# Kernel optimization log

Measured on AMD Instinct MI355X. Metric: run time of the kernel, lower is better.

## Reference

```python
import jax, jax.numpy as jnp
import numpy as np

B, N_IMG, D = 256, 128, 768
E, S, H = 3, 44, 1024  # S = ceil(128/3) rounded up to multiple of 4; H = 4*D//E
MAX_SLOTS = 88
LN_EPS = 1e-5


def setup_inputs() -> dict:
    key = jax.random.key(0)
    ks = jax.random.split(key, 12)
    x = jax.random.normal(ks[0], (B, N_IMG + 1, D), dtype=jnp.float32)
    attn_weight = jax.random.uniform(ks[1], (B, N_IMG), dtype=jnp.float32)
    ln_gamma = jnp.ones((D,), jnp.float32)
    ln_beta = jnp.zeros((D,), jnp.float32)
    vsg_w = jax.random.normal(ks[2], (D + 1, D), jnp.float32) / np.sqrt(D + 1)
    vsg_b = jnp.zeros((D,), jnp.float32)
    mu = jax.random.normal(ks[3], (E, D, MAX_SLOTS), jnp.float32) / np.sqrt(D)
    scale = jnp.ones((1,), jnp.float32)
    # per-expert MLP: kaiming-ish / xavier-ish random params
    w1 = jax.random.normal(ks[4], (E, D, H), jnp.float32) * np.sqrt(2.0 / D)
    b1 = jnp.zeros((E, H), jnp.float32)
    w2 = jax.random.normal(ks[5], (E, H, D), jnp.float32) * np.sqrt(2.0 / (H + D))
    b2 = jnp.zeros((E, D), jnp.float32)
    cw1 = jax.random.normal(ks[6], (D, 4 * D), jnp.float32) * np.sqrt(2.0 / D)
    cb1 = jnp.zeros((4 * D,), jnp.float32)
    cw2 = jax.random.normal(ks[7], (4 * D, D), jnp.float32) * np.sqrt(2.0 / (4 * D))
    cb2 = jnp.zeros((D,), jnp.float32)
    return dict(x=x, attn_weight=attn_weight, ln_gamma=ln_gamma, ln_beta=ln_beta,
                vsg_w=vsg_w, vsg_b=vsg_b, mu=mu, scale=scale,
                w1=w1, b1=b1, w2=w2, b2=b2, cw1=cw1, cb1=cb1, cw2=cw2, cb2=cb2)


def reference(x, attn_weight, ln_gamma, ln_beta, vsg_w, vsg_b, mu, scale,
              w1, b1, w2, b2, cw1, cb1, cw2, cb2):
    b, np1, d = x.shape
    n = np1 - 1
    img = x[:, 1:, :]            # [B, N, D]
    cls = x[:, 0, :]             # [B, D]

    # LayerNorm on image tokens
    mean = img.mean(-1, keepdims=True)
    var = img.var(-1, keepdims=True)  # biased, matches torch LayerNorm
    img_n = (img - mean) * jax.lax.rsqrt(var + LN_EPS) * ln_gamma + ln_beta

    # slot bias from [cls_feat, mean attention] -> visible_slot_gen (mode='original')
    attn_feat = attn_weight.mean(axis=1, keepdims=True)            # [B, 1]
    slot_input = jnp.concatenate([cls, attn_feat], axis=-1)        # [B, D+1]
    slot_bias = slot_input @ vsg_w + vsg_b                         # [B, D]

    # adjusted slot prototypes: mu[:, :, :S].permute(1,0,2) + slot_bias broadcast over (E, S)
    adj_mu = mu[:, :, :S].transpose(1, 0, 2)[None] + slot_bias[:, :, None, None]  # [B, D, E, S]

    logits = jnp.einsum('bnd,bdes->bnes', img_n * scale, adj_mu)   # [B, N, E, S]

    # expert group mask from attention thresholds (groups (1,1,1))
    vis = attn_weight > 0.7
    part = (attn_weight >= 0.3) & (attn_weight <= 0.7)
    occ = attn_weight < 0.3
    emask = jnp.stack([vis, part, occ], axis=-1).astype(logits.dtype)  # [B, N, E]
    logits = logits * emask[:, :, :, None]

    # softmax over tokens (dispatch) and over flattened slots (combine)
    dispatch = jax.nn.softmax(logits, axis=1)                      # [B, N, E, S]
    combine = jax.nn.softmax(logits.reshape(b, n, E * S), axis=-1) # [B, N, E*S]

    slot_in = jnp.einsum('bnd,bnes->besd', img, dispatch)          # [B, E, S, D]

    # batched per-expert MLP (fused grouped GEMM instead of python loop)
    h = jax.nn.gelu(jnp.einsum('besd,edh->besh', slot_in, w1) + b1[:, None, :],
                    approximate=False)
    slot_out = jnp.einsum('besh,ehd->besd', h, w2) + b2[:, None, :]  # [B, E, S, D]

    slot_flat = slot_out.reshape(b, E * S, d)
    img_out = jnp.einsum('bsd,bns->bnd', slot_flat, combine)       # [B, N, D]

    # CLS token through its dedicated dense MLP
    cls_h = jax.nn.gelu(cls @ cw1 + cb1, approximate=False)
    cls_out = cls_h @ cw2 + cb2                                    # [B, D]

    return jnp.concatenate([cls_out[:, None, :], img_out], axis=1)  # [B, N+1, D]
```

## Files before the change

### kernel.cpp

```cpp
#include <hip/hip_runtime.h>
#include <hip/hip_bf16.h>
#include <math.h>

#define NB   256
#define NIMG 128
#define DIM  768
#define NE   3
#define NS   44
#define NH   1024
#define ESL  132
#define NTOK (NB*NIMG)
#define MAXSLOTS 88
#define BIGI (1 << 30)
#define KPAD 160

typedef __bf16 bf16x8 __attribute__((ext_vector_type(8)));
typedef float f32x4 __attribute__((ext_vector_type(4)));
typedef const __attribute__((address_space(1))) void* gas_t;
typedef __attribute__((address_space(3))) void* las_t;

__device__ __forceinline__ float gelu_f(float v) {
    return 0.5f * v * (1.0f + erff(v * 0.70710678118654752f));
}

__device__ __forceinline__ float block_reduce_sum256(float v, float* red) {
    int tid = threadIdx.x;
    red[tid] = v;
    __syncthreads();
    for (int s = 128; s > 0; s >>= 1) {
        if (tid < s) red[tid] += red[tid + s];
        __syncthreads();
    }
    float r = red[0];
    __syncthreads();
    return r;
}

__global__ void repack_mu_k(const float* __restrict__ mu, __hip_bfloat16* __restrict__ bt) {
    int idx = blockIdx.x * 256 + threadIdx.x;
    if (idx >= 256 * DIM) return;
    int r = idx / DIM, d = idx - r * DIM;
    float v = 0.f;
    if (r < ESL) {
        int e = r / NS, s = r - e * NS;
        v = mu[((size_t)e * DIM + d) * MAXSLOTS + s];
    }
    bt[idx] = __float2bfloat16(v);
}

__global__ void transpose_bf16_k(const float* __restrict__ in, __hip_bfloat16* __restrict__ outp,
                                 int R, int Cc, long long inBS, long long outBS) {
    __shared__ float t[32][33];
    in   += (long long)blockIdx.z * inBS;
    outp += (long long)blockIdx.z * outBS;
    int c0 = blockIdx.x * 32, r0 = blockIdx.y * 32;
    int tx = threadIdx.x, ty = threadIdx.y;
    for (int i = 0; i < 32; i += 8) {
        int r = r0 + ty + i, c = c0 + tx;
        t[ty + i][tx] = (r < R && c < Cc) ? in[(size_t)r * Cc + c] : 0.f;
    }
    __syncthreads();
    for (int i = 0; i < 32; i += 8) {
        int r = c0 + ty + i, c = r0 + tx;
        if (r < Cc && c < R) outp[(size_t)r * R + c] = __float2bfloat16(t[tx][ty + i]);
    }
}

__global__ void cls_bf16_k(const float* __restrict__ x, __hip_bfloat16* __restrict__ cls16) {
    int idx = blockIdx.x * 256 + threadIdx.x;
    if (idx >= NB * DIM) return;
    int b = idx / DIM, j = idx - b * DIM;
    cls16[idx] = __float2bfloat16(x[(size_t)b * 129 * DIM + j]);
}

__global__ void zero_pad_k(__hip_bfloat16* __restrict__ p) {
    const int per = KPAD - ESL;
    const int total = NB * DIM * per;
    int idx = blockIdx.x * 256 + threadIdx.x;
    if (idx >= total) return;
    int bd = idx / per, k = idx - bd * per;
    p[(size_t)bd * KPAD + ESL + k] = __float2bfloat16(0.f);
}

__global__ void slot_bias_k(const float* __restrict__ x, const float* __restrict__ aw,
                            const float* __restrict__ vsg_w, const float* __restrict__ vsg_b,
                            float* __restrict__ slot_bias) {
    __shared__ float red[256];
    __shared__ float cls[DIM];
    int b = blockIdx.x, tid = threadIdx.x;
    float a = (tid < NIMG) ? aw[b * NIMG + tid] : 0.f;
    float af = block_reduce_sum256(a, red) * (1.0f / NIMG);
    for (int j = tid; j < DIM; j += 256) cls[j] = x[(size_t)b * 129 * DIM + j];
    __syncthreads();
    int j0 = tid, j1 = tid + 256, j2 = tid + 512;
    float acc0 = 0.f, acc1 = 0.f, acc2 = 0.f;
    for (int d = 0; d < DIM; ++d) {
        float c = cls[d];
        const float* wr = vsg_w + (size_t)d * DIM;
        acc0 = fmaf(c, wr[j0], acc0);
        acc1 = fmaf(c, wr[j1], acc1);
        acc2 = fmaf(c, wr[j2], acc2);
    }
    const float* wl = vsg_w + (size_t)DIM * DIM;
    float* out = slot_bias + (size_t)b * DIM;
    out[j0] = acc0 + vsg_b[j0] + af * wl[j0];
    out[j1] = acc1 + vsg_b[j1] + af * wl[j1];
    out[j2] = acc2 + vsg_b[j2] + af * wl[j2];
}

__global__ void ln_t2_k(const float* __restrict__ x, const float* __restrict__ gamma,
                        const float* __restrict__ beta, const float* __restrict__ slot_bias,
                        __hip_bfloat16* __restrict__ img_n, float* __restrict__ t2) {
    __shared__ float red[256];
    int tok = blockIdx.x;
    int b = tok >> 7, n = tok & 127;
    int tid = threadIdx.x;
    const float* row = x + ((size_t)b * 129 + 1 + n) * DIM;
    float v0 = row[tid], v1 = row[tid + 256], v2 = row[tid + 512];
    float s  = block_reduce_sum256(v0 + v1 + v2, red);
    float ss = block_reduce_sum256(v0*v0 + v1*v1 + v2*v2, red);
    float mean = s * (1.0f / DIM);
    float var  = ss * (1.0f / DIM) - mean * mean;
    float inv  = rsqrtf(var + 1e-5f);
    const float* sb = slot_bias + (size_t)b * DIM;
    __hip_bfloat16* orow = img_n + (size_t)tok * DIM;
    float tacc = 0.f;
    int j = tid;
    float y0 = (v0 - mean) * inv * gamma[j] + beta[j]; orow[j] = __float2bfloat16(y0); tacc = fmaf(y0, sb[j], tacc);
    j = tid + 256;
    float y1 = (v1 - mean) * inv * gamma[j] + beta[j]; orow[j] = __float2bfloat16(y1); tacc = fmaf(y1, sb[j], tacc);
    j = tid + 512;
    float y2 = (v2 - mean) * inv * gamma[j] + beta[j]; orow[j] = __float2bfloat16(y2); tacc = fmaf(y2, sb[j], tacc);
    float t = block_reduce_sum256(tacc, red);
    if (tid == 0) t2[tok] = t;
}

__global__ void mask_k(float* __restrict__ L, const float* __restrict__ t2,
                       const float* __restrict__ aw, const float* __restrict__ scale) {
    int idx = blockIdx.x * 256 + threadIdx.x;
    if (idx >= NTOK * ESL) return;
    int tok = idx / ESL, r = idx - tok * ESL;
    int e = r / NS;
    float a = aw[tok];
    int sel = (a > 0.7f) ? 0 : ((a >= 0.3f) ? 1 : 2);
    float v = 0.f;
    if (e == sel) v = scale[0] * (L[idx] + t2[tok]);
    L[idx] = v;
}

__global__ void dispatch_k(const float* __restrict__ L, __hip_bfloat16* __restrict__ dT16) {
    __shared__ float red[128];
    int es = blockIdx.x, b = blockIdx.y, tid = threadIdx.x;
    float v = L[((size_t)(b * NIMG + tid)) * ESL + es];
    red[tid] = v; __syncthreads();
    for (int s = 64; s > 0; s >>= 1) { if (tid < s) red[tid] = fmaxf(red[tid], red[tid + s]); __syncthreads(); }
    float mx = red[0]; __syncthreads();
    float e = __expf(v - mx);
    red[tid] = e; __syncthreads();
    for (int s = 64; s > 0; s >>= 1) { if (tid < s) red[tid] += red[tid + s]; __syncthreads(); }
    float sum = red[0];
    dT16[((size_t)b * ESL + es) * NIMG + tid] = __float2bfloat16(e / sum);
}

__global__ void combine_k(const float* __restrict__ L, __hip_bfloat16* __restrict__ C) {
    int tok = blockIdx.x, lane = threadIdx.x;
    const float* row = L + (size_t)tok * ESL;
    float v0 = row[lane], v1 = row[lane + 64];
    bool has2 = lane < (ESL - 128);
    float v2 = has2 ? row[lane + 128] : -1e30f;
    float m = fmaxf(fmaxf(v0, v1), v2);
    for (int o = 32; o > 0; o >>= 1) m = fmaxf(m, __shfl_xor(m, o));
    float e0 = __expf(v0 - m), e1 = __expf(v1 - m);
    float e2 = has2 ? __expf(v2 - m) : 0.f;
    float s = e0 + e1 + e2;
    for (int o = 32; o > 0; o >>= 1) s += __shfl_xor(s, o);
    float inv = 1.0f / s;
    __hip_bfloat16* orow = C + (size_t)tok * KPAD;
    orow[lane] = __float2bfloat16(e0 * inv);
    orow[lane + 64] = __float2bfloat16(e1 * inv);
    if (has2) orow[lane + 128] = __float2bfloat16(e2 * inv);
    else if (lane < KPAD - 128) orow[lane + 128] = __float2bfloat16(0.f);
}

__global__ __launch_bounds__(256)
void mfma2_k(const __hip_bfloat16* __restrict__ A_, long long aBS, int lda, int Mrows,
             const __hip_bfloat16* __restrict__ Bt_, long long bBS, int ldb, int Nrows,
             const float* __restrict__ bias, long long biasBS,
             void* __restrict__ Cv, long long cBS, int ldc, int cSub, long long cOuter,
             int Mlim, int Nlim, int K, int act, int out_bf16, int ctrans,
             int nx, int ny, int order)
{
    int nwg = gridDim.x;
    int hw = blockIdx.x;
    int q = nwg >> 3, r = nwg & 7;
    int xcd = hw & 7, off0 = hw >> 3;
    int wid = (xcd < r ? xcd * (q + 1) : r * (q + 1) + (xcd - r) * q) + off0;
    int pp = nx * ny;
    int bz = wid / pp;
    int rm = wid - bz * pp;
    int bx, by;
    if (order == 0) { by = rm / nx; bx = rm - by * nx; }
    else            { bx = rm / ny; by = rm - bx * ny; }

    const unsigned short* A  = (const unsigned short*)A_  + (long long)bz * aBS;
    const unsigned short* Bt = (const unsigned short*)Bt_ + (long long)bz * bBS;
    if (bias) bias += (long long)bz * biasBS;
    long long cbase = (long long)bz * cBS;

    __shared__ unsigned short As[2][128 * 32];
    __shared__ unsigned short Bs[2][128 * 32];

    int tid = threadIdx.x;
    int lane = tid & 63, wv = tid >> 6;
    int m0 = by * 128, n0 = bx * 128;

    const unsigned short* ga[2];
    const unsigned short* gb[2];
    int ldsoff[2];
#pragma unroll
    for (int i = 0; i < 2; ++i) {
        int j = wv * 2 + i;
        int p = j * 64 + lane;
        int rr = p >> 2;
        int cg = (p & 3) ^ ((rr >> 1) & 3);
        int ra = m0 + rr; if (ra > Mrows - 1) ra = Mrows - 1;
        int rb = n0 + rr; if (rb > Nrows - 1) rb = Nrows - 1;
        ga[i] = A  + (long long)ra * lda + cg * 8;
        gb[i] = Bt + (long long)rb * ldb + cg * 8;
        ldsoff[i] = j * 512;
    }

    int lrow = lane & 15, quad = lane >> 4;
    int wm = (wv >> 1) * 64, wn = (wv & 1) * 64;
    int offA[4], offB[4];
#pragma unroll
    for (int i = 0; i < 4; ++i) {
        int rowa = wm + i * 16 + lrow;
        offA[i] = rowa * 32 + ((quad ^ ((rowa >> 1) & 3)) * 8);
        int rowb = wn + i * 16 + lrow;
        offB[i] = rowb * 32 + ((quad ^ ((rowb >> 1) & 3)) * 8);
    }

    f32x4 acc[4][4] = {};
    int nt = K >> 5;

#pragma unroll
    for (int i = 0; i < 2; ++i) {
        __builtin_amdgcn_global_load_lds((gas_t)(ga[i]), (las_t)(&As[0][0] + ldsoff[i]), 16, 0, 0);
        __builtin_amdgcn_global_load_lds((gas_t)(gb[i]), (las_t)(&Bs[0][0] + ldsoff[i]), 16, 0, 0);
    }

    for (int t = 0; t < nt; ++t) {
        int cur = t & 1;
        if (t + 1 < nt) {
            int k0 = (t + 1) << 5;
            int nxt = cur ^ 1;
#pragma unroll
            for (int i = 0; i < 2; ++i) {
                __builtin_amdgcn_global_load_lds((gas_t)(ga[i] + k0), (las_t)(&As[nxt][0] + ldsoff[i]), 16, 0, 0);
                __builtin_amdgcn_global_load_lds((gas_t)(gb[i] + k0), (las_t)(&Bs[nxt][0] + ldsoff[i]), 16, 0, 0);
            }
            asm volatile("s_waitcnt vmcnt(4)" ::: "memory");
        } else {
            asm volatile("s_waitcnt vmcnt(0)" ::: "memory");
        }
        __builtin_amdgcn_s_barrier();
        bf16x8 af[4], bfr[4];
#pragma unroll
        for (int i = 0; i < 4; ++i) {
            af[i]  = *(const bf16x8*)(&As[cur][0] + offA[i]);
            bfr[i] = *(const bf16x8*)(&Bs[cur][0] + offB[i]);
        }
#pragma unroll
        for (int i = 0; i < 4; ++i)
#pragma unroll
            for (int j = 0; j < 4; ++j)
                acc[i][j] = __builtin_amdgcn_mfma_f32_16x16x32_bf16(af[i], bfr[j], acc[i][j], 0, 0, 0);
        if (t + 1 < nt) {
            asm volatile("s_waitcnt lgkmcnt(0)" ::: "memory");
            __builtin_amdgcn_s_barrier();
        }
    }

    float* Cf = (float*)Cv;
    __hip_bfloat16* Cb = (__hip_bfloat16*)Cv;
    if (ctrans == 2) {
        long long cb2[4]; int cols[4];
#pragma unroll
        for (int ni = 0; ni < 4; ++ni) {
            int col = n0 + wn + ni * 16 + lrow;
            cols[ni] = col;
            int qq = col / cSub, sl = col - qq * cSub;
            cb2[ni] = cbase + (long long)qq * cOuter + sl;
        }
#pragma unroll
        for (int mi = 0; mi < 4; ++mi) {
#pragma unroll
            for (int rr = 0; rr < 4; ++rr) {
                int row = m0 + wm + mi * 16 + quad * 4 + rr;
                if (row >= Mlim) continue;
                float bv = bias ? bias[row] : 0.f;
                long long rb = (long long)row * ldc;
#pragma unroll
                for (int ni = 0; ni < 4; ++ni) {
                    if (cols[ni] < Nlim) {
                        float v = acc[mi][ni][rr] + bv;
                        if (act == 1) v = gelu_f(v);
                        long long off = cb2[ni] + rb;
                        if (out_bf16) Cb[off] = __float2bfloat16(v);
                        else          Cf[off] = v;
                    }
                }
            }
        }
    } else {
#pragma unroll
        for (int mi = 0; mi < 4; ++mi) {
#pragma unroll
            for (int rr = 0; rr < 4; ++rr) {
                int row = m0 + wm + mi * 16 + quad * 4 + rr;
                if (row >= Mlim) continue;
                int qq = row / cSub;
                int sl = row - qq * cSub;
                long long rb = ctrans ? (cbase + (long long)qq * cOuter + sl)
                                      : (cbase + ((long long)qq * cOuter + sl) * ldc);
#pragma unroll
                for (int ni = 0; ni < 4; ++ni) {
                    int col = n0 + wn + ni * 16 + lrow;
                    if (col < Nlim) {
                        float v = acc[mi][ni][rr];
                        if (bias) v += bias[col];
                        if (act == 1) v = gelu_f(v);
                        long long off = ctrans ? (rb + (long long)col * ldc) : (rb + col);
                        if (out_bf16) Cb[off] = __float2bfloat16(v);
                        else          Cf[off] = v;
                    }
                }
            }
        }
    }
}

static inline void mfma2(hipStream_t st, int nx, int ny, int nz, int order,
                         const void* A, long long aBS, int lda, int Mrows,
                         const void* Bt, long long bBS, int ldb, int Nrows,
                         const float* bias, long long biasBS,
                         void* C, long long cBS, int ldc, int cSub, long long cOuter,
                         int Mlim, int Nlim, int K, int act, int obf, int ct) {
    mfma2_k<<<nx * ny * nz, dim3(256), 0, st>>>((const __hip_bfloat16*)A, aBS, lda, Mrows,
                                        (const __hip_bfloat16*)Bt, bBS, ldb, Nrows,
                                        bias, biasBS, C, cBS, ldc, cSub, cOuter,
                                        Mlim, Nlim, K, act, obf, ct, nx, ny, order);
}

extern "C" void kernel_launch(void* const* d_in, const int* in_sizes, int n_in,
                              void* d_out, int out_size, void* d_ws, size_t ws_size,
                              hipStream_t stream) {
    const float* x     = (const float*)d_in[0];
    const float* aw    = (const float*)d_in[1];
    const float* gamma = (const float*)d_in[2];
    const float* beta  = (const float*)d_in[3];
    const float* vsg_w = (const float*)d_in[4];
    const float* vsg_b = (const float*)d_in[5];
    const float* mu    = (const float*)d_in[6];
    const float* scale = (const float*)d_in[7];
    const float* w1    = (const float*)d_in[8];
    const float* b1    = (const float*)d_in[9];
    const float* w2    = (const float*)d_in[10];
    const float* b2    = (const float*)d_in[11];
    const float* cw1   = (const float*)d_in[12];
    const float* cb1   = (const float*)d_in[13];
    const float* cw2   = (const float*)d_in[14];
    const float* cb2   = (const float*)d_in[15];
    float* out = (float*)d_out;

    float* ws = (float*)d_ws;

    const long long IMGN_FL = (long long)NTOK * DIM / 2;
    const long long LOG_FL  = (long long)NTOK * ESL;
    const long long REG1_FL = (long long)NE * NB * NS * NH / 2;
    __hip_bfloat16* img_n = (__hip_bfloat16*)ws;
    float* logits = ws + IMGN_FL;
    __hip_bfloat16* h = (__hip_bfloat16*)ws;
    long long o = REG1_FL;
    __hip_bfloat16* dT16    = (__hip_bfloat16*)(ws + o); o += (long long)NB * ESL * NIMG / 2;
    __hip_bfloat16* comb_p  = (__hip_bfloat16*)(ws + o); o += (long long)NTOK * KPAD / 2;
    __hip_bfloat16* imgT    = (__hip_bfloat16*)(ws + o);
    __hip_bfloat16* slot_outT = imgT;                    o += (long long)NB * DIM * KPAD / 2;
    __hip_bfloat16* slot_in = (__hip_bfloat16*)(ws + o); o += (long long)NE * NB * NS * DIM / 2;
    __hip_bfloat16* mu_p    = (__hip_bfloat16*)(ws + o); o += 256 * DIM / 2;
    float* slot_bias = ws + o;                           o += NB * DIM;
    float* t2        = ws + o;                           o += NTOK;
    __hip_bfloat16* w1t  = (__hip_bfloat16*)(ws + o);    o += (long long)NE * NH * DIM / 2;
    __hip_bfloat16* w2t  = (__hip_bfloat16*)(ws + o);    o += (long long)NE * DIM * NH / 2;
    __hip_bfloat16* cw1t = (__hip_bfloat16*)(ws + o);    o += (long long)4 * DIM * DIM / 2;
    __hip_bfloat16* cw2t = (__hip_bfloat16*)(ws + o);    o += (long long)4 * DIM * DIM / 2;
    __hip_bfloat16* cls16 = (__hip_bfloat16*)(ws + o);   o += NB * DIM / 2;
    __hip_bfloat16* cls_h = (__hip_bfloat16*)(ws + o);   o += (long long)NB * 4 * DIM / 2;

    repack_mu_k<<<(256 * DIM + 255) / 256, 256, 0, stream>>>(mu, mu_p);
    transpose_bf16_k<<<dim3(NH / 32, DIM / 32, NE), dim3(32, 8), 0, stream>>>(w1, w1t, DIM, NH, (long long)DIM * NH, (long long)NH * DIM);
    transpose_bf16_k<<<dim3(DIM / 32, NH / 32, NE), dim3(32, 8), 0, stream>>>(w2, w2t, NH, DIM, (long long)NH * DIM, (long long)DIM * NH);
    transpose_bf16_k<<<dim3(4 * DIM / 32, DIM / 32, 1), dim3(32, 8), 0, stream>>>(cw1, cw1t, DIM, 4 * DIM, 0, 0);
    transpose_bf16_k<<<dim3(DIM / 32, 4 * DIM / 32, 1), dim3(32, 8), 0, stream>>>(cw2, cw2t, 4 * DIM, DIM, 0, 0);
    cls_bf16_k<<<(NB * DIM + 255) / 256, 256, 0, stream>>>(x, cls16);
    transpose_bf16_k<<<dim3(DIM / 32, NIMG / 32, NB), dim3(32, 8), 0, stream>>>(x + DIM, imgT, NIMG, DIM, (long long)129 * DIM, (long long)DIM * NIMG);

    slot_bias_k<<<NB, 256, 0, stream>>>(x, aw, vsg_w, vsg_b, slot_bias);
    ln_t2_k<<<NTOK, 256, 0, stream>>>(x, gamma, beta, slot_bias, img_n, t2);

    mfma2(stream, 2, NTOK / 128, 1, 0,
          img_n, 0, DIM, NTOK, mu_p, 0, DIM, 256, nullptr, 0,
          logits, 0, ESL, BIGI, 0, NTOK, ESL, DIM, 0, 0, 0);

    mask_k<<<(NTOK * ESL + 255) / 256, 256, 0, stream>>>(logits, t2, aw, scale);
    dispatch_k<<<dim3(ESL, NB), 128, 0, stream>>>(logits, dT16);
    combine_k<<<NTOK, 64, 0, stream>>>(logits, comb_p);

    mfma2(stream, DIM / 128, 2, NB, 0,
          dT16, (long long)ESL * NIMG, NIMG, ESL,
          imgT, (long long)DIM * NIMG, NIMG, DIM, nullptr, 0,
          slot_in, (long long)NS * DIM, DIM, NS, NB * NS,
          ESL, DIM, NIMG, 0, 1, 0);

    mfma2(stream, NH / 128, NB * NS / 128, NE, 0,
          slot_in, (long long)NB * NS * DIM, DIM, NB * NS,
          w1t, (long long)NH * DIM, DIM, NH, b1, NH,
          h, (long long)NB * NS * NH, NH, BIGI, 0,
          NB * NS, NH, DIM, 1, 1, 0);

    zero_pad_k<<<(NB * DIM * (KPAD - ESL) + 255) / 256, 256, 0, stream>>>(slot_outT);

    mfma2(stream, NB * NS / 128, DIM / 128, NE, 1,
          w2t, (long long)DIM * NH, NH, DIM,
          h, (long long)NB * NS * NH, NH, NB * NS,
          b2, DIM,
          slot_outT, NS, KPAD, NS, (long long)DIM * KPAD,
          DIM, NB * NS, NH, 0, 1, 2);

    mfma2(stream, DIM / 128, 1, NB, 0,
          comb_p, (long long)NIMG * KPAD, KPAD, NIMG,
          slot_outT, (long long)DIM * KPAD, KPAD, DIM, nullptr, 0,
          out + DIM, (long long)129 * DIM, DIM, BIGI, 0,
          NIMG, DIM, KPAD, 0, 0, 0);

    mfma2(stream, 4 * DIM / 128, NB / 128, 1, 0,
          cls16, 0, DIM, NB, cw1t, 0, DIM, 4 * DIM, cb1, 0,
          cls_h, 0, 4 * DIM, BIGI, 0, NB, 4 * DIM, DIM, 1, 1, 0);
    mfma2(stream, DIM / 128, NB / 128, 1, 0,
          cls_h, 0, 4 * DIM, NB, cw2t, 0, 4 * DIM, DIM, cb2, 0,
          out, 0, DIM, 1, 129, NB, DIM, 4 * DIM, 0, 0, 0);
}
```

Baseline: 925.0 us.

## Fuse mask and both softmaxes per batch; triple-buffer GEMM LDS to drop a barrier

Replaces the separate mask, dispatch-softmax and combine-softmax kernels with one kernel per batch. That kernel loads the batch's logits tile into shared memory once, applies the expert mask, and computes both the row softmax and the column softmax from LDS. The goal is to avoid rewriting and rereading the full logits buffer across three launches. The GEMM kernel also moves from double to triple-buffered LDS tiles, which lets it drop the trailing barrier in each k-iteration. The costs are lower parallelism (256 blocks, with serial per-thread loops and strided, uncoalesced bf16 stores), more LDS per block, and larger shared-memory use in the GEMM, which may reduce occupancy.

```diff
diff --git a/kernel.cpp b/kernel.cpp
--- a/kernel.cpp
+++ b/kernel.cpp
@@ -135,51 +135,47 @@
     if (tid == 0) t2[tok] = t;
 }
 
-__global__ void mask_k(float* __restrict__ L, const float* __restrict__ t2,
-                       const float* __restrict__ aw, const float* __restrict__ scale) {
-    int idx = blockIdx.x * 256 + threadIdx.x;
-    if (idx >= NTOK * ESL) return;
-    int tok = idx / ESL, r = idx - tok * ESL;
-    int e = r / NS;
-    float a = aw[tok];
-    int sel = (a > 0.7f) ? 0 : ((a >= 0.3f) ? 1 : 2);
-    float v = 0.f;
-    if (e == sel) v = scale[0] * (L[idx] + t2[tok]);
-    L[idx] = v;
-}
-
-__global__ void dispatch_k(const float* __restrict__ L, __hip_bfloat16* __restrict__ dT16) {
-    __shared__ float red[128];
-    int es = blockIdx.x, b = blockIdx.y, tid = threadIdx.x;
-    float v = L[((size_t)(b * NIMG + tid)) * ESL + es];
-    red[tid] = v; __syncthreads();
-    for (int s = 64; s > 0; s >>= 1) { if (tid < s) red[tid] = fmaxf(red[tid], red[tid + s]); __syncthreads(); }
-    float mx = red[0]; __syncthreads();
-    float e = __expf(v - mx);
-    red[tid] = e; __syncthreads();
-    for (int s = 64; s > 0; s >>= 1) { if (tid < s) red[tid] += red[tid + s]; __syncthreads(); }
-    float sum = red[0];
-    dT16[((size_t)b * ESL + es) * NIMG + tid] = __float2bfloat16(e / sum);
-}
-
-__global__ void combine_k(const float* __restrict__ L, __hip_bfloat16* __restrict__ C) {
-    int tok = blockIdx.x, lane = threadIdx.x;
-    const float* row = L + (size_t)tok * ESL;
-    float v0 = row[lane], v1 = row[lane + 64];
-    bool has2 = lane < (ESL - 128);
-    float v2 = has2 ? row[lane + 128] : -1e30f;
-    float m = fmaxf(fmaxf(v0, v1), v2);
-    for (int o = 32; o > 0; o >>= 1) m = fmaxf(m, __shfl_xor(m, o));
-    float e0 = __expf(v0 - m), e1 = __expf(v1 - m);
-    float e2 = has2 ? __expf(v2 - m) : 0.f;
-    float s = e0 + e1 + e2;
-    for (int o = 32; o > 0; o >>= 1) s += __shfl_xor(s, o);
-    float inv = 1.0f / s;
-    __hip_bfloat16* orow = C + (size_t)tok * KPAD;
-    orow[lane] = __float2bfloat16(e0 * inv);
-    orow[lane + 64] = __float2bfloat16(e1 * inv);
-    if (has2) orow[lane + 128] = __float2bfloat16(e2 * inv);
-    else if (lane < KPAD - 128) orow[lane + 128] = __float2bfloat16(0.f);
+__global__ __launch_bounds__(256)
+void softmax_fused_k(const float* __restrict__ L, const float* __restrict__ t2,
+                     const float* __restrict__ aw, const float* __restrict__ scale,
+                     __hip_bfloat16* __restrict__ dT16, __hip_bfloat16* __restrict__ C) {
+    __shared__ float Ls[NIMG][ESL + 1];
+    __shared__ float awS[NIMG], t2S[NIMG];
+    int b = blockIdx.x, tid = threadIdx.x;
+    if (tid < NIMG) { awS[tid] = aw[b * NIMG + tid]; t2S[tid] = t2[b * NIMG + tid]; }
+    __syncthreads();
+    float sc = scale[0];
+    const float* Lb = L + (size_t)b * NIMG * ESL;
+    for (int i = tid; i < NIMG * ESL; i += 256) {
+        int n = i / ESL, r = i - n * ESL;
+        int e = r / NS;
+        float a = awS[n];
+        int sel = (a > 0.7f) ? 0 : ((a >= 0.3f) ? 1 : 2);
+        Ls[n][r] = (e == sel) ? sc * (Lb[i] + t2S[n]) : 0.f;
+    }
+    __syncthreads();
+    if (tid < NIMG) {
+        int n = tid;
+        float m = -1e30f;
+        for (int r = 0; r < ESL; ++r) m = fmaxf(m, Ls[n][r]);
+        float s = 0.f;
+        for (int r = 0; r < ESL; ++r) s += __expf(Ls[n][r] - m);
+        float inv = 1.0f / s;
+        __hip_bfloat16* orow = C + ((size_t)b * NIMG + n) * KPAD;
+        for (int r = 0; r < ESL; ++r) orow[r] = __float2bfloat16(__expf(Ls[n][r] - m) * inv);
+        for (int r = ESL; r < KPAD; ++r) orow[r] = __float2bfloat16(0.f);
+    }
+    __syncthreads();
+    if (tid < ESL) {
+        int es = tid;
+        float m = -1e30f;
+        for (int n = 0; n < NIMG; ++n) m = fmaxf(m, Ls[n][es]);
+        float s = 0.f;
+        for (int n = 0; n < NIMG; ++n) { float e = __expf(Ls[n][es] - m); Ls[n][es] = e; s += e; }
+        float inv = 1.0f / s;
+        __hip_bfloat16* orow = dT16 + ((size_t)b * ESL + es) * NIMG;
+        for (int n = 0; n < NIMG; ++n) orow[n] = __float2bfloat16(Ls[n][es] * inv);
+    }
 }
 
 __global__ __launch_bounds__(256)
@@ -207,8 +203,8 @@
     if (bias) bias += (long long)bz * biasBS;
     long long cbase = (long long)bz * cBS;
 
-    __shared__ unsigned short As[2][128 * 32];
-    __shared__ unsigned short Bs[2][128 * 32];
+    __shared__ unsigned short As[3][128 * 32];
+    __shared__ unsigned short Bs[3][128 * 32];
 
     int tid = threadIdx.x;
     int lane = tid & 63, wv = tid >> 6;
@@ -250,11 +246,11 @@
         __builtin_amdgcn_global_load_lds((gas_t)(gb[i]), (las_t)(&Bs[0][0] + ldsoff[i]), 16, 0, 0);
     }
 
+    int cur = 0;
     for (int t = 0; t < nt; ++t) {
-        int cur = t & 1;
+        int nxt = (cur == 2) ? 0 : cur + 1;
         if (t + 1 < nt) {
             int k0 = (t + 1) << 5;
-            int nxt = cur ^ 1;
 #pragma unroll
             for (int i = 0; i < 2; ++i) {
                 __builtin_amdgcn_global_load_lds((gas_t)(ga[i] + k0), (las_t)(&As[nxt][0] + ldsoff[i]), 16, 0, 0);
@@ -276,10 +272,8 @@
 #pragma unroll
             for (int j = 0; j < 4; ++j)
                 acc[i][j] = __builtin_amdgcn_mfma_f32_16x16x32_bf16(af[i], bfr[j], acc[i][j], 0, 0, 0);
-        if (t + 1 < nt) {
-            asm volatile("s_waitcnt lgkmcnt(0)" ::: "memory");
-            __builtin_amdgcn_s_barrier();
-        }
+        asm volatile("s_waitcnt lgkmcnt(0)" ::: "memory");
+        cur = nxt;
     }
 
     float* Cf = (float*)Cv;
@@ -377,7 +371,6 @@
     float* ws = (float*)d_ws;
 
     const long long IMGN_FL = (long long)NTOK * DIM / 2;
-    const long long LOG_FL  = (long long)NTOK * ESL;
     const long long REG1_FL = (long long)NE * NB * NS * NH / 2;
     __hip_bfloat16* img_n = (__hip_bfloat16*)ws;
     float* logits = ws + IMGN_FL;
@@ -413,9 +406,7 @@
           img_n, 0, DIM, NTOK, mu_p, 0, DIM, 256, nullptr, 0,
           logits, 0, ESL, BIGI, 0, NTOK, ESL, DIM, 0, 0, 0);
 
-    mask_k<<<(NTOK * ESL + 255) / 256, 256, 0, stream>>>(logits, t2, aw, scale);
-    dispatch_k<<<dim3(ESL, NB), 128, 0, stream>>>(logits, dT16);
-    combine_k<<<NTOK, 64, 0, stream>>>(logits, comb_p);
+    softmax_fused_k<<<NB, 256, 0, stream>>>(logits, t2, aw, scale, dT16, comb_p);
 
     mfma2(stream, DIM / 128, 2, NB, 0,
           dT16, (long long)ESL * NIMG, NIMG, ESL,
```

Result: faster. 898.5 us (-2.9%).
